# Optimization experiments

Hardware: AMD Instinct MI355X
Metric: run time of the kernel (lower is better)

## Reference

```python
import jax, jax.numpy as jnp
import numpy as np

C = 32           # max_channels (in == out == 32, stride 1)
K = 3            # base kernel size
EXP_NITER = 5    # ConvExponential iterations -> effective kernel 11x11
POWER_IT = 3     # FantasticFour power iterations
B, H, W = 16, 256, 256


def _l2n(x):
    # L2Normalize over all dims (applied on store via right_inverse and again on read; idempotent)
    return x / (jnp.sqrt(jnp.sum(x * x)) + 1e-12)


def _skew(k):
    # K - flip(K^T, spatial)
    return k - jnp.flip(jnp.transpose(k, (1, 0, 2, 3)), axis=(2, 3))


def _fantastic_four(kernel, u1, u2, u3, u4):
    u1, u2, u3, u4 = map(_l2n, (u1, u2, u3, u4))
    for _ in range(POWER_IT):
        v1 = _l2n(jnp.sum(kernel * u1, axis=(1, 3), keepdims=True))
        u1 = _l2n(jnp.sum(kernel * v1, axis=(0, 2), keepdims=True))
        v2 = _l2n(jnp.sum(kernel * u2, axis=(1, 2), keepdims=True))
        u2 = _l2n(jnp.sum(kernel * v2, axis=(0, 3), keepdims=True))
        v3 = _l2n(jnp.sum(kernel * u3, axis=(1, 2, 3), keepdims=True))
        u3 = _l2n(jnp.sum(kernel * v3, axis=0, keepdims=True))
        v4 = _l2n(jnp.sum(kernel * u4, axis=(0, 2, 3), keepdims=True))
        u4 = _l2n(jnp.sum(kernel * v4, axis=1, keepdims=True))
    sg = jax.lax.stop_gradient  # sigmas use detached u/v, grad only via kernel
    s1 = jnp.sum(kernel * sg(u1) * sg(v1))
    s2 = jnp.sum(kernel * sg(u2) * sg(v2))
    s3 = jnp.sum(kernel * sg(u3) * sg(v3))
    s4 = jnp.sum(kernel * sg(u4) * sg(v4))
    sigma = jnp.minimum(jnp.minimum(s1, s2), jnp.minimum(s3, s4))
    return kernel / sigma


def _conv_exp(kernel):
    # kernel_global = I + K + K*K/2! + ... (kernel composition = full spatial convolution)
    p = (K - 1) // 2
    ident = jnp.pad(jnp.eye(C, dtype=kernel.dtype)[:, :, None, None],
                    ((0, 0), (0, 0), (p, p), (p, p)))
    kg = kernel + ident            # (C, C, K, K)
    ki = kernel
    rhs = jnp.flip(kernel, axis=(2, 3))  # flip -> lax correlation becomes full convolution
    for i in range(2, EXP_NITER + 1):
        # out[o,d,y,x] = sum_{c,p,q} ki[c,d,y-p,x-q] * kernel[o,c,p,q]
        inp = jnp.transpose(ki, (1, 0, 2, 3))  # (d, c, h, w) as NCHW
        out = jax.lax.conv_general_dilated(
            inp, rhs, window_strides=(1, 1),
            padding=[(K - 1, K - 1), (K - 1, K - 1)],
            dimension_numbers=('NCHW', 'OIHW', 'NCHW'))
        ki = jnp.transpose(out, (1, 0, 2, 3)) / float(i)
        kg = jnp.pad(kg, ((0, 0), (0, 0), (p, p), (p, p))) + ki
    return kg  # (C, C, 11, 11) for K=3, EXP_NITER=5


def reference(x, weight_raw, bias, u1, u2, u3, u4):
    w = _conv_exp(_fantastic_four(_skew(weight_raw), u1, u2, u3, u4))
    pad = w.shape[2] // 2  # 5
    z = jnp.pad(x, ((0, 0), (0, 0), (pad, pad), (pad, pad)), mode='wrap')  # circular
    z = jax.lax.conv_general_dilated(
        z, w, window_strides=(1, 1), padding='VALID',
        dimension_numbers=('NCHW', 'OIHW', 'NCHW'))
    return z + bias[None, :, None, None]


def setup_inputs() -> dict:
    key = jax.random.key(0)
    ks = jax.random.split(key, 7)
    return {
        'x': jax.random.normal(ks[0], (B, C, H, W), dtype=jnp.float32),
        'weight_raw': jax.random.normal(ks[1], (C, C, K, K), dtype=jnp.float32),
        'bias': jax.random.normal(ks[2], (C,), dtype=jnp.float32),
        'u1': jax.random.normal(ks[3], (1, C, 1, K), dtype=jnp.float32),
        'u2': jax.random.normal(ks[4], (1, C, K, 1), dtype=jnp.float32),
        'u3': jax.random.normal(ks[5], (1, C, K, K), dtype=jnp.float32),
        'u4': jax.random.normal(ks[6], (C, 1, K, K), dtype=jnp.float32),
    }
```

## Files before the change

kernel.cpp:

```cpp
#include <hip/hip_runtime.h>
#include <math.h>

typedef __bf16 bf16x8 __attribute__((ext_vector_type(8)));
typedef float f32x16 __attribute__((ext_vector_type(16)));
typedef unsigned int uint4v __attribute__((ext_vector_type(4)));

__device__ __forceinline__ unsigned short bf16_rne(float f) {
    unsigned u = __float_as_uint(f);
    unsigned r = u + 0x7fffu + ((u >> 16) & 1u);
    return (unsigned short)(r >> 16);
}
__device__ __forceinline__ float bf16_to_f(unsigned short h) {
    return __uint_as_float(((unsigned)h) << 16);
}

__device__ __forceinline__ float block_sum256(float v, float* red) {
    #pragma unroll
    for (int off = 32; off > 0; off >>= 1)
        v += __shfl_down(v, off, 64);
    const int tid = threadIdx.x;
    if ((tid & 63) == 0) red[tid >> 6] = v;
    __syncthreads();
    float tot = red[0] + red[1] + red[2] + red[3];
    __syncthreads();
    return tot;
}

__device__ __forceinline__ void l2n_lds(float* a, int n, float* red) {
    float s = 0.f;
    for (int i = threadIdx.x; i < n; i += 256) s += a[i] * a[i];
    const float tot = block_sum256(s, red);
    const float sc = 1.0f / (sqrtf(tot) + 1e-12f);
    for (int i = threadIdx.x; i < n; i += 256) a[i] *= sc;
    __syncthreads();
}

__global__ __launch_bounds__(256) void ff_kernel(
    const float* __restrict__ wr,
    const float* __restrict__ u1g, const float* __restrict__ u2g,
    const float* __restrict__ u3g, const float* __restrict__ u4g,
    float* __restrict__ kf_out)
{
    __shared__ float ks[9216];
    __shared__ float u1[96], v1[96], u2[96], v2[96];
    __shared__ float u3[288], u4[288], v3[32], v4[32];
    __shared__ float red[8];
    const int tid = threadIdx.x;

    for (int i = tid; i < 9216; i += 256) {
        int q  = i % 3;
        int p  = (i / 3) % 3;
        int ic = (i / 9) % 32;
        int oc = i / 288;
        ks[i] = wr[i] - wr[ic * 288 + oc * 9 + (2 - p) * 3 + (2 - q)];
    }
    if (tid < 96) { u1[tid] = u1g[tid]; u2[tid] = u2g[tid]; }
    for (int i = tid; i < 288; i += 256) { u3[i] = u3g[i]; u4[i] = u4g[i]; }
    __syncthreads();
    l2n_lds(u1, 96, red);
    l2n_lds(u2, 96, red);
    l2n_lds(u3, 288, red);
    l2n_lds(u4, 288, red);

    for (int it = 0; it < 3; ++it) {
        if (tid < 96) {
            int o = tid / 3, p = tid % 3;
            float s = 0.f;
            for (int i = 0; i < 32; ++i)
                for (int q = 0; q < 3; ++q)
                    s += ks[o * 288 + i * 9 + p * 3 + q] * u1[i * 3 + q];
            v1[tid] = s;
        }
        __syncthreads();
        l2n_lds(v1, 96, red);
        if (tid < 96) {
            int i = tid / 3, q = tid % 3;
            float s = 0.f;
            for (int o = 0; o < 32; ++o)
                for (int p = 0; p < 3; ++p)
                    s += ks[o * 288 + i * 9 + p * 3 + q] * v1[o * 3 + p];
            u1[tid] = s;
        }
        __syncthreads();
        l2n_lds(u1, 96, red);
        if (tid < 96) {
            int o = tid / 3, q = tid % 3;
            float s = 0.f;
            for (int i = 0; i < 32; ++i)
                for (int p = 0; p < 3; ++p)
                    s += ks[o * 288 + i * 9 + p * 3 + q] * u2[i * 3 + p];
            v2[tid] = s;
        }
        __syncthreads();
        l2n_lds(v2, 96, red);
        if (tid < 96) {
            int i = tid / 3, p = tid % 3;
            float s = 0.f;
            for (int o = 0; o < 32; ++o)
                for (int q = 0; q < 3; ++q)
                    s += ks[o * 288 + i * 9 + p * 3 + q] * v2[o * 3 + q];
            u2[tid] = s;
        }
        __syncthreads();
        l2n_lds(u2, 96, red);
        if (tid < 32) {
            float s = 0.f;
            for (int i = 0; i < 32; ++i)
                for (int pq = 0; pq < 9; ++pq)
                    s += ks[tid * 288 + i * 9 + pq] * u3[i * 9 + pq];
            v3[tid] = s;
        }
        __syncthreads();
        l2n_lds(v3, 32, red);
        for (int j = tid; j < 288; j += 256) {
            float s = 0.f;
            for (int o = 0; o < 32; ++o)
                s += ks[o * 288 + j] * v3[o];
            u3[j] = s;
        }
        __syncthreads();
        l2n_lds(u3, 288, red);
        if (tid < 32) {
            float s = 0.f;
            for (int o = 0; o < 32; ++o)
                for (int pq = 0; pq < 9; ++pq)
                    s += ks[o * 288 + tid * 9 + pq] * u4[o * 9 + pq];
            v4[tid] = s;
        }
        __syncthreads();
        l2n_lds(v4, 32, red);
        for (int j = tid; j < 288; j += 256) {
            int o = j / 9, pq = j - o * 9;
            float s = 0.f;
            for (int i = 0; i < 32; ++i)
                s += ks[o * 288 + i * 9 + pq] * v4[i];
            u4[j] = s;
        }
        __syncthreads();
        l2n_lds(u4, 288, red);
    }

    float p1 = 0.f, p2 = 0.f, p3 = 0.f, p4 = 0.f;
    for (int idx = tid; idx < 9216; idx += 256) {
        int q = idx % 3;
        int p = (idx / 3) % 3;
        int i = (idx / 9) % 32;
        int o = idx / 288;
        float k = ks[idx];
        p1 += k * u1[i * 3 + q] * v1[o * 3 + p];
        p2 += k * u2[i * 3 + p] * v2[o * 3 + q];
        p3 += k * u3[i * 9 + p * 3 + q] * v3[o];
        p4 += k * u4[o * 9 + p * 3 + q] * v4[i];
    }
    float s1 = block_sum256(p1, red);
    float s2 = block_sum256(p2, red);
    float s3 = block_sum256(p3, red);
    float s4 = block_sum256(p4, red);
    float sigma = fminf(fminf(s1, s2), fminf(s3, s4));
    for (int idx = tid; idx < 9216; idx += 256)
        kf_out[idx] = ks[idx] / sigma;
}

__global__ void initacc_kernel(const float* __restrict__ kf, float* __restrict__ wacc) {
    int idx = blockIdx.x * 256 + threadIdx.x;
    if (idx >= 123904) return;
    int o = idx / 3872;
    int rem = idx - o * 3872;
    int c = rem / 121;
    int yx = rem - c * 121;
    int y = yx / 11, x = yx - y * 11;
    float v = (o == c && y == 5 && x == 5) ? 1.0f : 0.0f;
    if (y >= 4 && y <= 6 && x >= 4 && x <= 6)
        v += kf[o * 288 + c * 9 + (y - 4) * 3 + (x - 4)];
    wacc[idx] = v;
}

__global__ void expstep_kernel(const float* __restrict__ kf, const float* __restrict__ ki,
                               float* __restrict__ ko, float* __restrict__ wacc,
                               int S, float scale)
{
    const int S2 = S + 2;
    const int off = (11 - S2) >> 1;
    const int o = blockIdx.x >> 5;
    const int d = blockIdx.x & 31;
    for (int yx = threadIdx.x; yx < S2 * S2; yx += blockDim.x) {
        int y = yx / S2, xx = yx - y * S2;
        float s = 0.f;
        for (int c = 0; c < 32; ++c) {
            const float* kfo = kf + o * 288 + c * 9;
            const float* kic = ki + (c * 32 + d) * S * S;
            #pragma unroll
            for (int p = 0; p < 3; ++p) {
                int yy = y - p;
                if (yy < 0 || yy >= S) continue;
                #pragma unroll
                for (int q = 0; q < 3; ++q) {
                    int xq = xx - q;
                    if (xq < 0 || xq >= S) continue;
                    s += kfo[p * 3 + q] * kic[yy * S + xq];
                }
            }
        }
        s *= scale;
        ko[(o * 32 + d) * S2 * S2 + yx] = s;
        wacc[(o * 32 + d) * 121 + (y + off) * 11 + (xx + off)] += s;
    }
}

__global__ void wprep_kernel(const float* __restrict__ wacc, uint4v* __restrict__ wbuf) {
    int idx = blockIdx.x * 256 + threadIdx.x;
    if (idx >= 30976) return;
    int lane  = idx & 63;
    int split = (idx >> 6) & 1;
    int ch    = (idx >> 7) & 1;
    int tap   = idx >> 8;
    int o     = lane & 31;
    int cbase = ch * 16 + ((lane >> 5) << 3);
    unsigned short v[8];
    #pragma unroll
    for (int j = 0; j < 8; ++j) {
        float w = wacc[o * 3872 + (cbase + j) * 121 + tap];
        unsigned short h = bf16_rne(w);
        v[j] = split ? bf16_rne(w - bf16_to_f(h)) : h;
    }
    uint4v u;
    u.x = (unsigned)v[0] | ((unsigned)v[1] << 16);
    u.y = (unsigned)v[2] | ((unsigned)v[3] << 16);
    u.z = (unsigned)v[4] | ((unsigned)v[5] << 16);
    u.w = (unsigned)v[6] | ((unsigned)v[7] << 16);
    wbuf[idx] = u;
}

__global__ __launch_bounds__(256, 2) void conv_mfma_kernel(
    const float* __restrict__ x, const uint4v* __restrict__ wbuf,
    const float* __restrict__ bias, float* __restrict__ out)
{
    __shared__ unsigned short shi[1092 * 16];
    __shared__ unsigned short slo[1092 * 16];
    __shared__ float biasS[32];

    const int b    = blockIdx.z;
    const int Y0   = blockIdx.y << 4;
    const int X0   = blockIdx.x << 5;
    const int tid  = threadIdx.x;
    const int lane = tid & 63;
    const int ywave = (tid >> 6) << 2;
    const int myoff = ((lane & 31) << 1) + (lane >> 5);

    if (tid < 32) biasS[tid] = bias[tid];

    f32x16 acc[4];
    #pragma unroll
    for (int s = 0; s < 4; ++s)
        #pragma unroll
        for (int r = 0; r < 16; ++r) acc[s][r] = 0.f;

    const uint4v* ph = (const uint4v*)shi;
    const uint4v* pl = (const uint4v*)slo;

    for (int chlf = 0; chlf < 2; ++chlf) {
        __syncthreads();
        const float* xb = x + (((size_t)(b * 32 + chlf * 16)) << 16);
        for (int pix = tid; pix < 1092; pix += 256) {
            int r = pix / 42, s = pix - r * 42;
            int gy = (Y0 + r - 5) & 255;
            int gx = (X0 + s - 5) & 255;
            const float* xp = xb + (gy << 8) + gx;
            unsigned short hv[16], lv[16];
            #pragma unroll
            for (int cc = 0; cc < 16; ++cc) {
                float v = xp[(size_t)cc << 16];
                unsigned short h = bf16_rne(v);
                hv[cc] = h;
                lv[cc] = bf16_rne(v - bf16_to_f(h));
            }
            uint4v u;
            u.x = (unsigned)hv[0] | ((unsigned)hv[1] << 16);
            u.y = (unsigned)hv[2] | ((unsigned)hv[3] << 16);
            u.z = (unsigned)hv[4] | ((unsigned)hv[5] << 16);
            u.w = (unsigned)hv[6] | ((unsigned)hv[7] << 16);
            *(uint4v*)&shi[pix * 16] = u;
            u.x = (unsigned)hv[8]  | ((unsigned)hv[9]  << 16);
            u.y = (unsigned)hv[10] | ((unsigned)hv[11] << 16);
            u.z = (unsigned)hv[12] | ((unsigned)hv[13] << 16);
            u.w = (unsigned)hv[14] | ((unsigned)hv[15] << 16);
            *(uint4v*)&shi[pix * 16 + 8] = u;
            u.x = (unsigned)lv[0] | ((unsigned)lv[1] << 16);
            u.y = (unsigned)lv[2] | ((unsigned)lv[3] << 16);
            u.z = (unsigned)lv[4] | ((unsigned)lv[5] << 16);
            u.w = (unsigned)lv[6] | ((unsigned)lv[7] << 16);
            *(uint4v*)&slo[pix * 16] = u;
            u.x = (unsigned)lv[8]  | ((unsigned)lv[9]  << 16);
            u.y = (unsigned)lv[10] | ((unsigned)lv[11] << 16);
            u.z = (unsigned)lv[12] | ((unsigned)lv[13] << 16);
            u.w = (unsigned)lv[14] | ((unsigned)lv[15] << 16);
            *(uint4v*)&slo[pix * 16 + 8] = u;
        }
        __syncthreads();

        const int wb0 = chlf * 128 + lane;
        uint4v a0 = wbuf[wb0];
        uint4v a1 = wbuf[wb0 + 64];
        #pragma unroll 1
        for (int tap = 0; tap < 121; ++tap) {
            bf16x8 Ahi = __builtin_bit_cast(bf16x8, a0);
            bf16x8 Alo = __builtin_bit_cast(bf16x8, a1);
            if (tap < 120) {
                a0 = wbuf[wb0 + (tap + 1) * 256];
                a1 = wbuf[wb0 + (tap + 1) * 256 + 64];
            }
            int p = tap / 11, q = tap - p * 11;
            int u0 = ((ywave + p) * 42 + q) * 2 + myoff;
            #pragma unroll
            for (int s = 0; s < 4; ++s) {
                bf16x8 Bh = __builtin_bit_cast(bf16x8, ph[u0 + s * 84]);
                bf16x8 Bl = __builtin_bit_cast(bf16x8, pl[u0 + s * 84]);
                acc[s] = __builtin_amdgcn_mfma_f32_32x32x16_bf16(Ahi, Bh, acc[s], 0, 0, 0);
                acc[s] = __builtin_amdgcn_mfma_f32_32x32x16_bf16(Alo, Bh, acc[s], 0, 0, 0);
                acc[s] = __builtin_amdgcn_mfma_f32_32x32x16_bf16(Ahi, Bl, acc[s], 0, 0, 0);
            }
        }
    }

    const int colx = X0 + (lane & 31);
    const int half = lane >> 5;
    #pragma unroll
    for (int s = 0; s < 4; ++s) {
        int y = Y0 + ywave + s;
        #pragma unroll
        for (int r = 0; r < 16; ++r) {
            int o = (r & 3) + ((r >> 2) << 3) + (half << 2);
            out[(((size_t)(b * 32 + o)) << 16) + (y << 8) + colx] = acc[s][r] + biasS[o];
        }
    }
}

extern "C" void kernel_launch(void* const* d_in, const int* in_sizes, int n_in,
                              void* d_out, int out_size, void* d_ws, size_t ws_size,
                              hipStream_t stream) {
    const float* x    = (const float*)d_in[0];
    const float* wraw = (const float*)d_in[1];
    const float* bias = (const float*)d_in[2];
    const float* u1   = (const float*)d_in[3];
    const float* u2   = (const float*)d_in[4];
    const float* u3   = (const float*)d_in[5];
    const float* u4   = (const float*)d_in[6];
    float* out = (float*)d_out;

    float* ws   = (float*)d_ws;
    float* kf   = ws;
    float* bufA = kf + 9216;
    float* bufB = bufA + 123904;
    float* wacc = bufB + 123904;
    uint4v* wbuf = (uint4v*)(wacc + 123904);

    ff_kernel<<<1, 256, 0, stream>>>(wraw, u1, u2, u3, u4, kf);
    initacc_kernel<<<484, 256, 0, stream>>>(kf, wacc);
    expstep_kernel<<<1024, 128, 0, stream>>>(kf, kf,   bufA, wacc, 3, 0.5f);
    expstep_kernel<<<1024, 128, 0, stream>>>(kf, bufA, bufB, wacc, 5, 1.0f / 3.0f);
    expstep_kernel<<<1024, 128, 0, stream>>>(kf, bufB, bufA, wacc, 7, 0.25f);
    expstep_kernel<<<1024, 128, 0, stream>>>(kf, bufA, bufB, wacc, 9, 0.2f);
    wprep_kernel<<<121, 256, 0, stream>>>(wacc, wbuf);

    conv_mfma_kernel<<<dim3(8, 16, 16), 256, 0, stream>>>(x, wbuf, bias, out);
}
```

Baseline: 926.5 us.

## Reorder conv loop by column to reuse LDS input rows across kernel rows

```diff
diff --git a/kernel.cpp b/kernel.cpp
--- a/kernel.cpp
+++ b/kernel.cpp
@@ -235,8 +235,8 @@
     const float* __restrict__ x, const uint4v* __restrict__ wbuf,
     const float* __restrict__ bias, float* __restrict__ out)
 {
-    __shared__ unsigned short shi[1092 * 16];
-    __shared__ unsigned short slo[1092 * 16];
+    __shared__ unsigned short shi[2 * 1092 * 8];
+    __shared__ unsigned short slo[2 * 1092 * 8];
     __shared__ float biasS[32];
 
     const int b    = blockIdx.z;
@@ -245,7 +245,7 @@
     const int tid  = threadIdx.x;
     const int lane = tid & 63;
     const int ywave = (tid >> 6) << 2;
-    const int myoff = ((lane & 31) << 1) + (lane >> 5);
+    const int myoff = (lane & 31) + (lane >> 5) * 1092;
 
     if (tid < 32) biasS[tid] = bias[tid];
 
@@ -279,45 +279,53 @@
             u.y = (unsigned)hv[2] | ((unsigned)hv[3] << 16);
             u.z = (unsigned)hv[4] | ((unsigned)hv[5] << 16);
             u.w = (unsigned)hv[6] | ((unsigned)hv[7] << 16);
-            *(uint4v*)&shi[pix * 16] = u;
+            *(uint4v*)&shi[pix * 8] = u;
             u.x = (unsigned)hv[8]  | ((unsigned)hv[9]  << 16);
             u.y = (unsigned)hv[10] | ((unsigned)hv[11] << 16);
             u.z = (unsigned)hv[12] | ((unsigned)hv[13] << 16);
             u.w = (unsigned)hv[14] | ((unsigned)hv[15] << 16);
-            *(uint4v*)&shi[pix * 16 + 8] = u;
+            *(uint4v*)&shi[(1092 + pix) * 8] = u;
             u.x = (unsigned)lv[0] | ((unsigned)lv[1] << 16);
             u.y = (unsigned)lv[2] | ((unsigned)lv[3] << 16);
             u.z = (unsigned)lv[4] | ((unsigned)lv[5] << 16);
             u.w = (unsigned)lv[6] | ((unsigned)lv[7] << 16);
-            *(uint4v*)&slo[pix * 16] = u;
+            *(uint4v*)&slo[pix * 8] = u;
             u.x = (unsigned)lv[8]  | ((unsigned)lv[9]  << 16);
             u.y = (unsigned)lv[10] | ((unsigned)lv[11] << 16);
             u.z = (unsigned)lv[12] | ((unsigned)lv[13] << 16);
             u.w = (unsigned)lv[14] | ((unsigned)lv[15] << 16);
-            *(uint4v*)&slo[pix * 16 + 8] = u;
+            *(uint4v*)&slo[(1092 + pix) * 8] = u;
         }
         __syncthreads();
 
         const int wb0 = chlf * 128 + lane;
-        uint4v a0 = wbuf[wb0];
-        uint4v a1 = wbuf[wb0 + 64];
         #pragma unroll 1
-        for (int tap = 0; tap < 121; ++tap) {
-            bf16x8 Ahi = __builtin_bit_cast(bf16x8, a0);
-            bf16x8 Alo = __builtin_bit_cast(bf16x8, a1);
-            if (tap < 120) {
-                a0 = wbuf[wb0 + (tap + 1) * 256];
-                a1 = wbuf[wb0 + (tap + 1) * 256 + 64];
-            }
-            int p = tap / 11, q = tap - p * 11;
-            int u0 = ((ywave + p) * 42 + q) * 2 + myoff;
+        for (int q = 0; q < 11; ++q) {
+            uint4v ah[8], al[8];
+            ah[0] = wbuf[wb0 + q * 256];
+            al[0] = wbuf[wb0 + q * 256 + 64];
+            ah[1] = wbuf[wb0 + (11 + q) * 256];
+            al[1] = wbuf[wb0 + (11 + q) * 256 + 64];
             #pragma unroll
-            for (int s = 0; s < 4; ++s) {
-                bf16x8 Bh = __builtin_bit_cast(bf16x8, ph[u0 + s * 84]);
-                bf16x8 Bl = __builtin_bit_cast(bf16x8, pl[u0 + s * 84]);
-                acc[s] = __builtin_amdgcn_mfma_f32_32x32x16_bf16(Ahi, Bh, acc[s], 0, 0, 0);
-                acc[s] = __builtin_amdgcn_mfma_f32_32x32x16_bf16(Alo, Bh, acc[s], 0, 0, 0);
-                acc[s] = __builtin_amdgcn_mfma_f32_32x32x16_bf16(Ahi, Bl, acc[s], 0, 0, 0);
+            for (int r = 0; r < 14; ++r) {
+                const int base = (ywave + r) * 42 + q + myoff;
+                bf16x8 Bh = __builtin_bit_cast(bf16x8, ph[base]);
+                bf16x8 Bl = __builtin_bit_cast(bf16x8, pl[base]);
+                const int plo = (r - 3 > 0) ? r - 3 : 0;
+                const int phi = (r < 10) ? r : 10;
+                #pragma unroll
+                for (int p = plo; p <= phi; ++p) {
+                    const int s = r - p;
+                    bf16x8 Ah = __builtin_bit_cast(bf16x8, ah[p & 7]);
+                    bf16x8 Al = __builtin_bit_cast(bf16x8, al[p & 7]);
+                    acc[s] = __builtin_amdgcn_mfma_f32_32x32x16_bf16(Ah, Bh, acc[s], 0, 0, 0);
+                    acc[s] = __builtin_amdgcn_mfma_f32_32x32x16_bf16(Al, Bh, acc[s], 0, 0, 0);
+                    acc[s] = __builtin_amdgcn_mfma_f32_32x32x16_bf16(Ah, Bl, acc[s], 0, 0, 0);
+                }
+                if (r + 2 <= 10) {
+                    ah[(r + 2) & 7] = wbuf[wb0 + ((r + 2) * 11 + q) * 256];
+                    al[(r + 2) & 7] = wbuf[wb0 + ((r + 2) * 11 + q) * 256 + 64];
+                }
             }
         }
     }
```

Result: no change. 929.0 us (+0.3%).
